# Optimization experiments

Measured on AMD Instinct MI355X. Metric: run time of the kernel, lower is better.

Reference implementation:

```python
import jax, jax.numpy as jnp
import numpy as np

# static config matching init_kwargs / setup
T = 0.1      # temperature
MARG = 0.0   # margin m
NEG_IOU = 0.5
K = 1        # pos_topk
WEIGHT = 1.0
P = 2080     # number of True entries in mask2d (triu of 64x64)


def _normalize(x, axis=-1, eps=1e-12):
    n = jnp.sqrt(jnp.sum(x * x, axis=axis, keepdims=True))
    return x / jnp.maximum(n, eps)


def _log_ce(pos_scores, all_scores, neg_mask, t, m):
    # pos_scores: (..., K); all_scores: (..., K or 1, L); neg_mask broadcastable to all_scores
    pos_logit = (pos_scores - m) / t
    pos_exp = jnp.exp(pos_logit)
    neg_exp_sum = jnp.sum(jnp.exp(all_scores / t) * neg_mask.astype(all_scores.dtype), axis=-1)
    loss = -(pos_logit - jnp.log(pos_exp + neg_exp_sum))
    return jnp.mean(loss)


def setup_inputs() -> dict:
    key = jax.random.key(0)
    k1, k2, k3, k4 = jax.random.split(key, 4)
    S, C, N, B, M = 64, 256, 64, 16, 128
    video_feats = jax.random.normal(k1, (S, C, N, N), dtype=jnp.float32)
    sents_feats = jax.random.normal(k2, (S, C), dtype=jnp.float32)
    iou2d = jax.random.uniform(k3, (S, N, N), dtype=jnp.float32)
    iou2ds = jax.random.uniform(k4, (M, N, N), dtype=jnp.float32)
    num_sentences = jnp.full((B,), 4, dtype=jnp.int32)   # sum == S
    num_targets = jnp.full((S,), 2, dtype=jnp.int32)     # sum == M
    mask2d = jnp.triu(jnp.ones((N, N), dtype=bool))      # P = 2080 valid proposals
    return {
        "video_feats": video_feats, "sents_feats": sents_feats,
        "iou2d": iou2d, "iou2ds": iou2ds,
        "num_sentences": num_sentences, "num_targets": num_targets,
        "mask2d": mask2d,
    }


def reference(video_feats, sents_feats, iou2d, iou2ds, num_sentences, num_targets, mask2d):
    S, C, N, _ = video_feats.shape
    B = num_sentences.shape[0]
    M = iou2ds.shape[0]

    # flat proposal indices (static count P)
    mask_idx = jnp.nonzero(mask2d.reshape(-1), size=P)[0]

    # scatter maps
    scatter_b2s = jnp.concatenate([jnp.zeros((1,), jnp.int32),
                                   jnp.cumsum(num_sentences)[:-1].astype(jnp.int32)])  # (B,)
    scatter_m2s = jnp.repeat(jnp.arange(S), num_targets, total_repeat_length=M)        # (M,)
    scatter_s2b = jnp.repeat(jnp.arange(B), num_sentences, total_repeat_length=S)      # (S,)

    # select valid proposals: (S,C,P) -> (S,P,C)
    vf = video_feats.reshape(S, C, N * N)[:, :, mask_idx].transpose(0, 2, 1)
    iou2d_f = iou2d.reshape(S, N * N)[:, mask_idx]    # (S,P)
    iou2ds_f = iou2ds.reshape(M, N * N)[:, mask_idx]  # (M,P)

    vf = _normalize(vf, axis=-1)          # (S,P,C)
    sf = _normalize(sents_feats, axis=-1) # (S,C)

    # top-K proposals per moment
    topk_idxs = jax.lax.top_k(iou2ds_f, K)[1]                         # (M,K)
    allm_vf = vf[scatter_m2s]                                         # (M,P,C)
    topk_vf = jnp.take_along_axis(allm_vf, topk_idxs[:, :, None], 1)  # (M,K,C)

    # inter-video loss
    inter_video_pos = jnp.sum(topk_vf * sf[scatter_m2s][:, None, :], axis=-1)  # (M,K)
    inter_video_all = jnp.einsum('mkc,sc->mks', topk_vf, sf)                   # (M,K,S)
    eye_mask = ~jnp.eye(S, dtype=bool)
    inter_video_neg_mask = eye_mask[scatter_m2s][:, None, :]                   # (M,1,S)
    loss_inter_video = _log_ce(inter_video_pos, inter_video_all, inter_video_neg_mask, T, MARG)

    # inter-query loss
    inter_query_pos = inter_video_pos                                  # (M,K)
    vf_b = vf[scatter_b2s].reshape(B * P, C)                           # one sentence-rep per video
    inter_query_all = jnp.einsum('sc,qc->sq', sf, vf_b)[:, None, :]    # (S,1,B*P)

    # pos_mask: row s has its video block b=scatter_s2b[s] set to (iou2d > neg_iou)
    s2v_pos = iou2d_f > NEG_IOU                                        # (S,P)
    pos_mask = jnp.zeros((S, B, P), dtype=bool)
    pos_mask = pos_mask.at[jnp.arange(S), scatter_s2b].set(s2v_pos)
    pos_mask = pos_mask.reshape(S, B * P)
    inter_query_neg_mask = (~pos_mask)[:, None, :]                     # (S,1,B*P)

    loss_inter_query = _log_ce(inter_query_pos,
                               inter_query_all[scatter_m2s],
                               inter_query_neg_mask[scatter_m2s], T, MARG)

    return (loss_inter_video + loss_inter_query) * WEIGHT
```

## Files before the change

### kernel.cpp

```cpp
#include <hip/hip_runtime.h>
#include <math.h>

#define C 256
#define NN 4096
#define T_INV 10.0f
#define NEG_IOU_TH 0.5f
#define SGROUP 8
#define FLATS 2
#define QTILES (NN / (256 * FLATS))

__device__ __forceinline__ float wave_reduce_sum(float v) {
    #pragma unroll
    for (int off = 32; off > 0; off >>= 1) v += __shfl_xor(v, off, 64);
    return v;
}

__global__ void k_prep(const float* __restrict__ sents,
                       const int* __restrict__ num_sentences,
                       const int* __restrict__ num_targets,
                       int B, int S, int M,
                       float* __restrict__ sfT, int* __restrict__ b2s,
                       int* __restrict__ s2b, int* __restrict__ m2s,
                       float* __restrict__ denomq, int* __restrict__ counter) {
    __shared__ float red[4];
    int s = blockIdx.x, tid = threadIdx.x;
    float v = sents[(size_t)s * C + tid];
    float ssq = wave_reduce_sum(v * v);
    int lane = tid & 63, wave = tid >> 6;
    if (lane == 0) red[wave] = ssq;
    __syncthreads();
    float tot = red[0] + red[1] + red[2] + red[3];
    sfT[(size_t)tid * S + s] = v * (1.0f / fmaxf(sqrtf(tot), 1e-12f));

    if (blockIdx.x == 0) {
        if (tid < S) denomq[tid] = 0.f;
        if (tid == 0) {
            *counter = 0;
            int acc = 0;
            for (int b = 0; b < B; ++b) {
                b2s[b] = acc;
                int nsb = num_sentences[b];
                for (int k = 0; k < nsb; ++k) s2b[acc + k] = b;
                acc += nsb;
            }
            int mi = 0;
            for (int si = 0; si < S; ++si) {
                int nt = num_targets[si];
                for (int k = 0; k < nt; ++k) m2s[mi++] = si;
            }
        }
    }
}

__global__ void __launch_bounds__(256)
k_main(const float* __restrict__ vf, const float* __restrict__ iou2d,
       const float* __restrict__ iou2ds, const int* __restrict__ num_sentences,
       const float* __restrict__ sfT, const int* __restrict__ b2s,
       const int* __restrict__ m2s,
       float* __restrict__ pos, float* __restrict__ negiv,
       float* __restrict__ denomq, int* __restrict__ counter,
       float* __restrict__ out, int S, int B, int M, int nq, int ntot) {
    __shared__ float smem[C * SGROUP];
    __shared__ float red[4];
    __shared__ int   sidx[4];
    __shared__ float dw[4][SGROUP];
    __shared__ int   bestflat;
    __shared__ int   amlast;

    int bid = blockIdx.x, tid = threadIdx.x;
    int lane = tid & 63, wave = tid >> 6;

    if (bid >= M) {
        int qb   = bid - M;
        int tile = qb % QTILES;
        int rem  = qb / QTILES;
        int b    = rem % B;
        int g    = rem / B;
        int sb = b2s[b];
        int ns = num_sentences[b];
        int s0 = g * SGROUP;

        for (int k = tid; k < C * SGROUP; k += 256) {
            int c = k / SGROUP, s = k % SGROUP;
            smem[k] = sfT[(size_t)c * S + s0 + s];
        }
        __syncthreads();

        int flat0 = tile * (256 * FLATS) + tid * FLATS;
        const float2* vp = (const float2*)(vf + (size_t)sb * C * NN + flat0);

        float2 acc[SGROUP];
        #pragma unroll
        for (int s = 0; s < SGROUP; ++s) acc[s] = make_float2(0.f, 0.f);
        float ssx = 0.f, ssy = 0.f;

        #pragma unroll 4
        for (int c = 0; c < C; ++c) {
            float2 v = vp[(size_t)c * (NN / 2)];
            ssx += v.x * v.x;
            ssy += v.y * v.y;
            const float4* sr = (const float4*)&smem[c * SGROUP];
            #pragma unroll
            for (int q = 0; q < SGROUP / 4; ++q) {
                float4 s4 = sr[q];
                acc[q*4+0].x += s4.x * v.x;  acc[q*4+0].y += s4.x * v.y;
                acc[q*4+1].x += s4.y * v.x;  acc[q*4+1].y += s4.y * v.y;
                acc[q*4+2].x += s4.z * v.x;  acc[q*4+2].y += s4.z * v.y;
                acc[q*4+3].x += s4.w * v.x;  acc[q*4+3].y += s4.w * v.y;
            }
        }

        int fA = flat0, fB = flat0 + 1;
        bool vA = ((fA & 63) >= (fA >> 6));
        bool vB = ((fB & 63) >= (fB >> 6));
        float invA = 1.0f / fmaxf(sqrtf(ssx), 1e-12f);
        float invB = 1.0f / fmaxf(sqrtf(ssy), 1e-12f);

        unsigned long long bitsA = 0ull, bitsB = 0ull;
        for (int i = 0; i < ns; ++i) {
            const float* row = iou2d + (size_t)(sb + i) * NN;
            if (vA && row[fA] > NEG_IOU_TH) bitsA |= (1ull << i);
            if (vB && row[fB] > NEG_IOU_TH) bitsB |= (1ull << i);
        }

        #pragma unroll
        for (int s = 0; s < SGROUP; ++s) {
            int s_abs = s0 + s;
            int rel = s_abs - sb;
            bool inblk = (rel >= 0 && rel < ns);
            float e = 0.f;
            if (vA && !(inblk && ((bitsA >> rel) & 1ull)))
                e += expf(acc[s].x * invA * T_INV);
            if (vB && !(inblk && ((bitsB >> rel) & 1ull)))
                e += expf(acc[s].y * invB * T_INV);
            e = wave_reduce_sum(e);
            if (lane == 0) dw[wave][s] = e;
        }
        __syncthreads();
        if (tid < SGROUP)
            atomicAdd(&denomq[s0 + tid],
                      dw[0][tid] + dw[1][tid] + dw[2][tid] + dw[3][tid]);
    } else {
        int m = bid;
        int s_m = m2s[m];
        float* tv  = smem;
        float* sc4 = smem + C;

        float bv = -1e30f; int bi = NN;
        #pragma unroll
        for (int j = 0; j < NN / 256; ++j) {
            int flat = tid + j * 256;
            int r = flat >> 6, cc = flat & 63;
            if (cc >= r) {
                float val = iou2ds[(size_t)m * NN + flat];
                if (val > bv || (val == bv && flat < bi)) { bv = val; bi = flat; }
            }
        }
        #pragma unroll
        for (int off = 32; off > 0; off >>= 1) {
            float ov = __shfl_xor(bv, off, 64);
            int   oi = __shfl_xor(bi, off, 64);
            if (ov > bv || (ov == bv && oi < bi)) { bv = ov; bi = oi; }
        }
        if (lane == 0) { red[wave] = bv; sidx[wave] = bi; }
        __syncthreads();
        if (tid == 0) {
            float v0 = red[0]; int i0 = sidx[0];
            for (int w = 1; w < 4; ++w)
                if (red[w] > v0 || (red[w] == v0 && sidx[w] < i0)) { v0 = red[w]; i0 = sidx[w]; }
            bestflat = i0;
        }
        __syncthreads();
        int flat = bestflat;

        float v = vf[((size_t)s_m * C + tid) * NN + flat];
        float ssq = wave_reduce_sum(v * v);
        if (lane == 0) red[wave] = ssq;
        __syncthreads();
        float tot = red[0] + red[1] + red[2] + red[3];
        tv[tid] = v * (1.0f / fmaxf(sqrtf(tot), 1e-12f));
        __syncthreads();

        {
            int s = tid & 63, cg = tid >> 6;
            float d = 0.f;
            for (int j = 0; j < 64; ++j) {
                int c2 = cg * 64 + j;
                d += tv[c2] * sfT[(size_t)c2 * S + s];
            }
            sc4[cg * 64 + s] = d;
        }
        __syncthreads();
        if (tid < 64) {
            float d = sc4[tid] + sc4[64 + tid] + sc4[128 + tid] + sc4[192 + tid];
            if (tid == s_m) atomicExch(&pos[m], d);
            float e = (tid == s_m) ? 0.f : expf(d * T_INV);
            e = wave_reduce_sum(e);
            if (tid == 0) atomicExch(&negiv[m], e);
        }
    }

    __syncthreads();
    if (tid == 0) {
        __threadfence();
        int old = atomicAdd(counter, 1);
        amlast = (old == ntot - 1) ? 1 : 0;
    }
    __syncthreads();
    if (!amlast) return;

    __threadfence();
    float val = 0.f;
    for (int m = tid; m < M; m += 256) {
        int s = m2s[m];
        float pl  = atomicAdd(&pos[m], 0.f) * T_INV;
        float niv = atomicAdd(&negiv[m], 0.f);
        float dq  = atomicAdd(&denomq[s], 0.f);
        float pe = expf(pl);
        val += -(pl - logf(pe + niv)) + -(pl - logf(pe + dq));
    }
    val = wave_reduce_sum(val);
    if (lane == 0) dw[0][wave] = val;
    __syncthreads();
    if (tid == 0) out[0] = (dw[0][0] + dw[0][1] + dw[0][2] + dw[0][3]) / (float)M;
}

extern "C" void kernel_launch(void* const* d_in, const int* in_sizes, int n_in,
                              void* d_out, int out_size, void* d_ws, size_t ws_size,
                              hipStream_t stream) {
    const float* video_feats   = (const float*)d_in[0];
    const float* sents_feats   = (const float*)d_in[1];
    const float* iou2d         = (const float*)d_in[2];
    const float* iou2ds        = (const float*)d_in[3];
    const int*   num_sentences = (const int*)d_in[4];
    const int*   num_targets   = (const int*)d_in[5];

    const int S = in_sizes[2] / NN;
    const int B = in_sizes[4];
    const int M = in_sizes[3] / NN;

    float* sfT    = (float*)d_ws;
    float* pos    = sfT + (size_t)C * 64;
    float* negiv  = pos + M;
    float* denomq = negiv + M;
    int*   b2s    = (int*)(denomq + S);
    int*   s2b    = b2s + B;
    int*   m2s    = s2b + S;
    int*   counter = m2s + M;

    const int nq   = QTILES * B * (S / SGROUP);
    const int ntot = M + nq;

    k_prep<<<S, C, 0, stream>>>(sents_feats, num_sentences, num_targets,
                                B, S, M, sfT, b2s, s2b, m2s, denomq, counter);
    k_main<<<ntot, 256, 0, stream>>>(video_feats, iou2d, iou2ds, num_sentences,
                                     sfT, b2s, m2s, pos, negiv, denomq, counter,
                                     (float*)d_out, S, B, M, nq, ntot);
}
```

Before: 383.5 us.

## Compute all 64 sentence scores per proposal tile to reuse video feature loads

The inter-query blocks now keep all 64 sentence vectors in shared memory and give each thread one proposal with 64 accumulators, where before each block handled 8 sentences and 2 proposals per thread. Each video feature element is read once instead of once per sentence group, cutting global memory traffic by the number of groups. The catch is heavy register pressure (64 accumulators), a 64 KB shared tile that lowers occupancy, far fewer blocks, and shape constants (S=64, B from qb>>4) hard-coded into the indexing.

```diff
diff --git a/kernel.cpp b/kernel.cpp
--- a/kernel.cpp
+++ b/kernel.cpp
@@ -3,11 +3,11 @@
 
 #define C 256
 #define NN 4096
+#define SDIM 64
 #define T_INV 10.0f
 #define NEG_IOU_TH 0.5f
-#define SGROUP 8
-#define FLATS 2
-#define QTILES (NN / (256 * FLATS))
+#define QTILE 256
+#define QTILES (NN / QTILE)
 
 __device__ __forceinline__ float wave_reduce_sum(float v) {
     #pragma unroll
@@ -60,10 +60,10 @@
        float* __restrict__ pos, float* __restrict__ negiv,
        float* __restrict__ denomq, int* __restrict__ counter,
        float* __restrict__ out, int S, int B, int M, int nq, int ntot) {
-    __shared__ float smem[C * SGROUP];
+    __shared__ float sT[C * SDIM];
     __shared__ float red[4];
     __shared__ int   sidx[4];
-    __shared__ float dw[4][SGROUP];
+    __shared__ float dw[4][SDIM];
     __shared__ int   bestflat;
     __shared__ int   amlast;
 
@@ -72,86 +72,81 @@
 
     if (bid >= M) {
         int qb   = bid - M;
-        int tile = qb % QTILES;
-        int rem  = qb / QTILES;
-        int b    = rem % B;
-        int g    = rem / B;
+        int tile = qb & (QTILES - 1);
+        int b    = qb >> 4;
         int sb = b2s[b];
         int ns = num_sentences[b];
-        int s0 = g * SGROUP;
-
-        for (int k = tid; k < C * SGROUP; k += 256) {
-            int c = k / SGROUP, s = k % SGROUP;
-            smem[k] = sfT[(size_t)c * S + s0 + s];
-        }
-        __syncthreads();
-
-        int flat0 = tile * (256 * FLATS) + tid * FLATS;
-        const float2* vp = (const float2*)(vf + (size_t)sb * C * NN + flat0);
-
-        float2 acc[SGROUP];
-        #pragma unroll
-        for (int s = 0; s < SGROUP; ++s) acc[s] = make_float2(0.f, 0.f);
-        float ssx = 0.f, ssy = 0.f;
-
-        #pragma unroll 4
-        for (int c = 0; c < C; ++c) {
-            float2 v = vp[(size_t)c * (NN / 2)];
-            ssx += v.x * v.x;
-            ssy += v.y * v.y;
-            const float4* sr = (const float4*)&smem[c * SGROUP];
+
+        {
+            const float4* src = (const float4*)sfT;
+            float4* dst = (float4*)sT;
             #pragma unroll
-            for (int q = 0; q < SGROUP / 4; ++q) {
-                float4 s4 = sr[q];
-                acc[q*4+0].x += s4.x * v.x;  acc[q*4+0].y += s4.x * v.y;
-                acc[q*4+1].x += s4.y * v.x;  acc[q*4+1].y += s4.y * v.y;
-                acc[q*4+2].x += s4.z * v.x;  acc[q*4+2].y += s4.z * v.y;
-                acc[q*4+3].x += s4.w * v.x;  acc[q*4+3].y += s4.w * v.y;
-            }
-        }
-
-        int fA = flat0, fB = flat0 + 1;
-        bool vA = ((fA & 63) >= (fA >> 6));
-        bool vB = ((fB & 63) >= (fB >> 6));
-        float invA = 1.0f / fmaxf(sqrtf(ssx), 1e-12f);
-        float invB = 1.0f / fmaxf(sqrtf(ssy), 1e-12f);
-
-        unsigned long long bitsA = 0ull, bitsB = 0ull;
-        for (int i = 0; i < ns; ++i) {
-            const float* row = iou2d + (size_t)(sb + i) * NN;
-            if (vA && row[fA] > NEG_IOU_TH) bitsA |= (1ull << i);
-            if (vB && row[fB] > NEG_IOU_TH) bitsB |= (1ull << i);
-        }
-
-        #pragma unroll
-        for (int s = 0; s < SGROUP; ++s) {
-            int s_abs = s0 + s;
-            int rel = s_abs - sb;
-            bool inblk = (rel >= 0 && rel < ns);
-            float e = 0.f;
-            if (vA && !(inblk && ((bitsA >> rel) & 1ull)))
-                e += expf(acc[s].x * invA * T_INV);
-            if (vB && !(inblk && ((bitsB >> rel) & 1ull)))
-                e += expf(acc[s].y * invB * T_INV);
+            for (int k = 0; k < (C * SDIM) / (4 * 256); ++k)
+                dst[tid + k * 256] = src[tid + k * 256];
+        }
+        __syncthreads();
+
+        int flat = tile * QTILE + tid;
+        const float* vp = vf + (size_t)sb * C * NN + flat;
+
+        float acc[SDIM];
+        #pragma unroll
+        for (int s = 0; s < SDIM; ++s) acc[s] = 0.f;
+        float ssq = 0.f;
+
+        for (int c0 = 0; c0 < C; c0 += 4) {
+            float v0 = vp[(size_t)(c0 + 0) * NN];
+            float v1 = vp[(size_t)(c0 + 1) * NN];
+            float v2 = vp[(size_t)(c0 + 2) * NN];
+            float v3 = vp[(size_t)(c0 + 3) * NN];
+            ssq += v0 * v0 + v1 * v1 + v2 * v2 + v3 * v3;
+            #pragma unroll
+            for (int j = 0; j < 4; ++j) {
+                float v = (j == 0) ? v0 : (j == 1) ? v1 : (j == 2) ? v2 : v3;
+                const float4* sr = (const float4*)&sT[(c0 + j) * SDIM];
+                #pragma unroll
+                for (int q4 = 0; q4 < SDIM / 4; ++q4) {
+                    float4 s4 = sr[q4];
+                    acc[q4 * 4 + 0] += s4.x * v;
+                    acc[q4 * 4 + 1] += s4.y * v;
+                    acc[q4 * 4 + 2] += s4.z * v;
+                    acc[q4 * 4 + 3] += s4.w * v;
+                }
+            }
+        }
+
+        int r = flat >> 6, cc = flat & 63;
+        bool valid = (cc >= r);
+        float scale = (1.0f / fmaxf(sqrtf(ssq), 1e-12f)) * T_INV;
+
+        unsigned long long excl = 0ull;
+        for (int i = 0; i < ns; ++i)
+            if (iou2d[(size_t)(sb + i) * NN + flat] > NEG_IOU_TH)
+                excl |= (1ull << (sb + i));
+        if (!valid) excl = ~0ull;
+
+        #pragma unroll
+        for (int s = 0; s < SDIM; ++s) {
+            float e = ((excl >> s) & 1ull) ? 0.f : expf(acc[s] * scale);
             e = wave_reduce_sum(e);
             if (lane == 0) dw[wave][s] = e;
         }
         __syncthreads();
-        if (tid < SGROUP)
-            atomicAdd(&denomq[s0 + tid],
+        if (tid < SDIM)
+            atomicAdd(&denomq[tid],
                       dw[0][tid] + dw[1][tid] + dw[2][tid] + dw[3][tid]);
     } else {
         int m = bid;
         int s_m = m2s[m];
-        float* tv  = smem;
-        float* sc4 = smem + C;
+        float* tv  = sT;
+        float* sc4 = sT + C;
 
         float bv = -1e30f; int bi = NN;
         #pragma unroll
         for (int j = 0; j < NN / 256; ++j) {
             int flat = tid + j * 256;
-            int r = flat >> 6, cc = flat & 63;
-            if (cc >= r) {
+            int rr = flat >> 6, cc = flat & 63;
+            if (cc >= rr) {
                 float val = iou2ds[(size_t)m * NN + flat];
                 if (val > bv || (val == bv && flat < bi)) { bv = val; bi = flat; }
             }
@@ -248,7 +243,7 @@
     int*   m2s    = s2b + S;
     int*   counter = m2s + M;
 
-    const int nq   = QTILES * B * (S / SGROUP);
+    const int nq   = QTILES * B;
     const int ntot = M + nq;
 
     k_prep<<<S, C, 0, stream>>>(sents_feats, num_sentences, num_targets,
```

Result: slower. 405.9 us (+5.8%).
